# Kernel tuning notes

Hardware: AMD Instinct MI355X
Metric: run time of the kernel (lower is better)

Reference implementation:

```python
import jax, jax.numpy as jnp
import numpy as np

EPS_F = 1e-12
M, N = 64, 4096  # feature dim m, num nodes n


def setup_inputs() -> dict:
    key = jax.random.key(0)
    k1, k2, k3, k4 = jax.random.split(key, 4)
    # X: (m, n) node features transposed, as in the repo (features.t())
    X = jax.random.normal(k1, (M, N), dtype=jnp.float32)
    # F: (m, m) parameter, xavier_uniform init
    bound = float(np.sqrt(6.0 / (M + M)))
    F = jax.random.uniform(k2, (M, M), minval=-bound, maxval=bound, dtype=jnp.float32)
    # Q_S: (n, n) orthogonal eigenvector matrix of the (symmetric, normalized) adjacency
    A = jax.random.normal(k3, (N, N), dtype=jnp.float32)
    Q_S, _ = jnp.linalg.qr(A)
    Q_S = Q_S.astype(jnp.float32)
    # Lambda_S: (n, 1) eigenvalues of normalized adjacency, inside (-1, 1)
    Lambda_S = jnp.sort(
        jax.random.uniform(k4, (N, 1), minval=-0.95, maxval=0.95, dtype=jnp.float32), axis=0
    )
    gamma = jnp.asarray(0.8, dtype=jnp.float32)
    return {"X": X, "F": F, "Q_S": Q_S, "Lambda_S": Lambda_S, "gamma": gamma}


def reference(X, F, Q_S, Lambda_S, gamma):
    # g(F) = F^T F / (||F^T F||_F + eps)  -- Frobenius-normalized Gram matrix
    FF = F.T @ F                                   # (m, m)
    G_F = FF / (jnp.linalg.norm(FF) + EPS_F)       # (m, m), symmetric PSD, ||.||_F ~ 1
    # spectral decomposition of g(F)
    Lambda_F, Q_F = jnp.linalg.eigh(G_F)           # (m,), (m, m)
    # closed-form equilibrium of Z = gamma * g(F) Z S^T + X in the joint eigenbasis
    D = 1.0 / (1.0 - gamma * Lambda_F[:, None] * Lambda_S.reshape(1, -1))  # (m, n)
    Z = Q_F @ (D * (Q_F.T @ X @ Q_S)) @ Q_S.T      # (m, n)
    return Z
```

## Files before the change

### kernel.cpp

```cpp
#include <hip/hip_runtime.h>
#include <math.h>


typedef short short8 __attribute__((ext_vector_type(8)));
typedef float floatx16 __attribute__((ext_vector_type(16)));

#define KSPLIT 16
#define KCHUNK 256
constexpr int Mdim = 64;
constexpr int Ndim = 4096;

__device__ inline ushort f2bf(float f) {
    uint u = __float_as_uint(f);
    u += 0x7fff + ((u >> 16) & 1);
    return (ushort)(u >> 16);
}
__device__ inline float bf2f(ushort h) { return __uint_as_float(((uint)h) << 16); }

__device__ inline floatx16 mfma_bf16(short8 a, short8 b, floatx16 c) {
    return __builtin_amdgcn_mfma_f32_32x32x16_bf16(a, b, c, 0, 0, 0);
}

struct SharedGemm { ushort Ah[4096], Al[4096], Bh[4096]; };
struct SharedPrep { float Fraw[64 * 65]; ushort Ph[4096], Pl[4096]; float red[256]; };
union SharedU { SharedGemm g; SharedPrep p; };

__global__ __launch_bounds__(256) void init_kernel(float* __restrict__ W, float* __restrict__ Z) {
    const int i = blockIdx.x * 256 + threadIdx.x;
    float4 z = {0.f, 0.f, 0.f, 0.f};
    if (i < 65536) *(float4*)&W[i * 4] = z;
    else *(float4*)&Z[(i - 65536) * 4] = z;
}

__device__ void prep_body(SharedPrep& sp, const float* __restrict__ F, float* __restrict__ Gout) {
    const int t = threadIdx.x;
    const int l = t & 63, w = t >> 6;
    const int tm = w & 1, tn = w >> 1;
    const int am = tm * 32 + (l & 31);
    const int bn = tn * 32 + (l & 31);
    const int lk = l >> 5;

    for (int s = 0; s < 4; ++s) {
        int e = t + 256 * s;
        int r = e >> 4, q = (e & 15) * 4;
        float4 v = *(const float4*)&F[r * 64 + q];
        float fa[4] = {v.x, v.y, v.z, v.w};
        for (int i = 0; i < 4; ++i) sp.Fraw[r * 65 + q + i] = fa[i];
    }
    __syncthreads();
    {
        int c = t >> 2, kbase = (t & 3) * 16;
        ushort hh[16], ll[16];
#pragma unroll
        for (int kk = 0; kk < 16; ++kk) {
            float v = sp.Fraw[(kbase + kk) * 65 + c];
            ushort h = f2bf(v);
            hh[kk] = h;
            ll[kk] = f2bf(v - bf2f(h));
        }
#pragma unroll
        for (int g = 0; g < 2; ++g) {
            int gk = (kbase >> 3) + g;
            int idx = c * 64 + ((gk ^ (c & 7)) * 8);
#pragma unroll
            for (int u = 0; u < 8; ++u) { sp.Ph[idx + u] = hh[8 * g + u]; sp.Pl[idx + u] = ll[8 * g + u]; }
        }
    }
    __syncthreads();
    floatx16 acc;
    for (int i = 0; i < 16; ++i) acc[i] = 0.f;
    for (int s16 = 0; s16 < 4; ++s16) {
        int gk = 2 * s16 + lk;
        int ai = am * 64 + ((gk ^ (am & 7)) * 8);
        int bi = bn * 64 + ((gk ^ (bn & 7)) * 8);
        short8 ah = *(const short8*)&sp.Ph[ai];
        short8 al = *(const short8*)&sp.Pl[ai];
        short8 bh = *(const short8*)&sp.Ph[bi];
        short8 bl = *(const short8*)&sp.Pl[bi];
        acc = mfma_bf16(ah, bh, acc);
        acc = mfma_bf16(al, bh, acc);
        acc = mfma_bf16(ah, bl, acc);
    }
    float ss = 0.f;
    for (int r = 0; r < 16; ++r) ss += acc[r] * acc[r];
    sp.red[t] = ss;
    __syncthreads();
    for (int off = 128; off > 0; off >>= 1) {
        if (t < off) sp.red[t] += sp.red[t + off];
        __syncthreads();
    }
    const float inv = 1.0f / (sqrtf(sp.red[0]) + 1e-12f);
    for (int r = 0; r < 16; ++r) {
        int row = (r & 3) + 8 * (r >> 2) + 4 * lk + tm * 32;
        int col = tn * 32 + (l & 31);
        float v = acc[r] * inv;
        Gout[row * 64 + col] = v;
        ushort h = f2bf(v);
        int idx = row * 64 + (((col >> 3) ^ (row & 7)) * 8 + (col & 7));
        sp.Ph[idx] = h;
        sp.Pl[idx] = f2bf(v - bf2f(h));
    }
    for (int j = 1; j < 5; ++j) {
        __syncthreads();
        floatx16 a2;
        for (int i = 0; i < 16; ++i) a2[i] = 0.f;
        for (int s16 = 0; s16 < 4; ++s16) {
            int gk = 2 * s16 + lk;
            int ai = am * 64 + ((gk ^ (am & 7)) * 8);
            int bi = bn * 64 + ((gk ^ (bn & 7)) * 8);
            short8 ah = *(const short8*)&sp.Ph[ai];
            short8 al = *(const short8*)&sp.Pl[ai];
            short8 bh = *(const short8*)&sp.Ph[bi];
            short8 bl = *(const short8*)&sp.Pl[bi];
            a2 = mfma_bf16(ah, bh, a2);
            a2 = mfma_bf16(al, bh, a2);
            a2 = mfma_bf16(ah, bl, a2);
        }
        __syncthreads();
        for (int r = 0; r < 16; ++r) {
            int row = (r & 3) + 8 * (r >> 2) + 4 * lk + tm * 32;
            int col = tn * 32 + (l & 31);
            float v = a2[r];
            Gout[j * 4096 + row * 64 + col] = v;
            ushort h = f2bf(v);
            int idx = row * 64 + (((col >> 3) ^ (row & 7)) * 8 + (col & 7));
            sp.Ph[idx] = h;
            sp.Pl[idx] = f2bf(v - bf2f(h));
        }
    }
}

template <bool TB, bool DOPREP>
__global__ __launch_bounds__(256, 4) void gemm_kernel(const float* __restrict__ A,
                                                      const float* __restrict__ Bm,
                                                      float* __restrict__ C,
                                                      const float* __restrict__ F,
                                                      float* __restrict__ Gp) {
    __shared__ SharedU sh;
    const int bid = blockIdx.x;
    if (DOPREP) {
        if (bid == 0) { prep_body(sh.p, F, Gp); return; }
    }
    const int b = DOPREP ? bid - 1 : bid;
    const int n0 = (b & 63) * 64;
    const int kb = (b >> 6) * KCHUNK;
    const int t = threadIdx.x;
    const int l = t & 63, w = t >> 6;
    const int tm = w & 1, tn = w >> 1;
    const int am = tm * 32 + (l & 31);
    const int bn = tn * 32 + (l & 31);
    const int lk = l >> 5;
    const int sr = t >> 2, sj = t & 3;
    const int nq = t & 15, kr2 = 2 * (t >> 4);

    floatx16 acc;
    for (int i = 0; i < 16; ++i) acc[i] = 0.f;

    float4 bbuf[2][4];
    if (TB) {
#pragma unroll
        for (int s = 0; s < 4; ++s)
            bbuf[0][s] = *(const float4*)&Bm[(size_t)(n0 + sr) * 4096 + kb + 4 * sj + 16 * s];
    } else {
#pragma unroll
        for (int s = 0; s < 2; ++s) {
            bbuf[0][2 * s + 0] = *(const float4*)&Bm[(size_t)(kb + kr2 + 32 * s) * 4096 + n0 + 4 * nq];
            bbuf[0][2 * s + 1] = *(const float4*)&Bm[(size_t)(kb + kr2 + 1 + 32 * s) * 4096 + n0 + 4 * nq];
        }
    }

#pragma unroll
    for (int step = 0; step < KCHUNK / 64; ++step) {
        const int k0 = kb + step * 64;
        const int cur = step & 1, nxt = cur ^ 1;
        float4 av[4];
#pragma unroll
        for (int s = 0; s < 4; ++s)
            av[s] = *(const float4*)&A[sr * 4096 + k0 + 4 * sj + 16 * s];
        __syncthreads();
        if (step + 1 < KCHUNK / 64) {
            const int k1 = k0 + 64;
            if (TB) {
#pragma unroll
                for (int s = 0; s < 4; ++s)
                    bbuf[nxt][s] = *(const float4*)&Bm[(size_t)(n0 + sr) * 4096 + k1 + 4 * sj + 16 * s];
            } else {
#pragma unroll
                for (int s = 0; s < 2; ++s) {
                    bbuf[nxt][2 * s + 0] = *(const float4*)&Bm[(size_t)(k1 + kr2 + 32 * s) * 4096 + n0 + 4 * nq];
                    bbuf[nxt][2 * s + 1] = *(const float4*)&Bm[(size_t)(k1 + kr2 + 1 + 32 * s) * 4096 + n0 + 4 * nq];
                }
            }
        }
        if (TB) {
#pragma unroll
            for (int s = 0; s < 4; ++s) {
                int off = 4 * sj + 16 * s;
                int idx = sr * 64 + (((off >> 3) ^ (sr & 7)) * 8 + (off & 7));
                float fb[4] = {bbuf[cur][s].x, bbuf[cur][s].y, bbuf[cur][s].z, bbuf[cur][s].w};
                ushort4 h4;
                ushort* hp = (ushort*)&h4;
#pragma unroll
                for (int i = 0; i < 4; ++i) hp[i] = f2bf(fb[i]);
                *(ushort4*)&sh.g.Bh[idx] = h4;
            }
        } else {
#pragma unroll
            for (int s = 0; s < 2; ++s) {
                int k = kr2 + 32 * s;
                float fa[4] = {bbuf[cur][2 * s].x, bbuf[cur][2 * s].y, bbuf[cur][2 * s].z, bbuf[cur][2 * s].w};
                float fb[4] = {bbuf[cur][2 * s + 1].x, bbuf[cur][2 * s + 1].y, bbuf[cur][2 * s + 1].z, bbuf[cur][2 * s + 1].w};
#pragma unroll
                for (int i = 0; i < 4; ++i) {
                    int n = 4 * nq + i;
                    int idx = n * 64 + (((k >> 3) ^ (n & 7)) * 8 + (k & 7));
                    ushort2 hp2;
                    hp2.x = f2bf(fa[i]);
                    hp2.y = f2bf(fb[i]);
                    *(ushort2*)&sh.g.Bh[idx] = hp2;
                }
            }
        }
#pragma unroll
        for (int s = 0; s < 4; ++s) {
            int off = 4 * sj + 16 * s;
            int idx = sr * 64 + (((off >> 3) ^ (sr & 7)) * 8 + (off & 7));
            float fa[4] = {av[s].x, av[s].y, av[s].z, av[s].w};
            ushort4 h4, l4;
            ushort* hp = (ushort*)&h4; ushort* lp = (ushort*)&l4;
#pragma unroll
            for (int i = 0; i < 4; ++i) {
                ushort h = f2bf(fa[i]);
                hp[i] = h; lp[i] = f2bf(fa[i] - bf2f(h));
            }
            *(ushort4*)&sh.g.Ah[idx] = h4;
            *(ushort4*)&sh.g.Al[idx] = l4;
        }
        __syncthreads();
#pragma unroll
        for (int s16 = 0; s16 < 4; ++s16) {
            int gk = 2 * s16 + lk;
            int ai = am * 64 + ((gk ^ (am & 7)) * 8);
            int bi = bn * 64 + ((gk ^ (bn & 7)) * 8);
            short8 ah = *(const short8*)&sh.g.Ah[ai];
            short8 al = *(const short8*)&sh.g.Al[ai];
            short8 bh = *(const short8*)&sh.g.Bh[bi];
            acc = mfma_bf16(ah, bh, acc);
            acc = mfma_bf16(al, bh, acc);
        }
    }
    const int colg = n0 + tn * 32 + (l & 31);
#pragma unroll
    for (int r = 0; r < 16; ++r) {
        int row = (r & 3) + 8 * (r >> 2) + 4 * lk + tm * 32;
        atomicAdd(&C[row * 4096 + colg], acc[r]);
    }
}

__global__ __launch_bounds__(256) void solve_kernel(const float* __restrict__ W,
                                                    const float* __restrict__ Gp,
                                                    const float* __restrict__ lam,
                                                    const float* __restrict__ gammap,
                                                    float* __restrict__ Y) {
    __shared__ float Gs[64][68];
    __shared__ float T[64][17];
    const int t = threadIdx.x;
    const int c0 = blockIdx.x * 16;
    for (int e = t; e < 1024; e += 256)
        T[e >> 4][e & 15] = W[(e >> 4) * 4096 + c0 + (e & 15)];
    const int tx = t & 15;
    const int r4 = (t >> 4) * 4;
    const float a = gammap[0] * lam[c0 + tx];
    float s = a;
    for (int j = 0; j < 5; ++j) {
        __syncthreads();
        for (int e = t; e < 4096; e += 256) Gs[e >> 6][e & 63] = Gp[j * 4096 + e];
        __syncthreads();
        float u0 = 0.f, u1 = 0.f, u2 = 0.f, u3 = 0.f;
#pragma unroll 8
        for (int k = 0; k < 64; ++k) {
            const float tv = T[k][tx];
            const float4 g = *(const float4*)&Gs[k][r4];
            u0 += g.x * tv; u1 += g.y * tv; u2 += g.z * tv; u3 += g.w * tv;
        }
        __syncthreads();
        T[r4 + 0][tx] += s * u0;
        T[r4 + 1][tx] += s * u1;
        T[r4 + 2][tx] += s * u2;
        T[r4 + 3][tx] += s * u3;
        s = s * s;
    }
    __syncthreads();
    for (int e = t; e < 1024; e += 256)
        Y[(e >> 4) * 4096 + c0 + (e & 15)] = T[e >> 4][e & 15];
}

extern "C" void kernel_launch(void* const* d_in, const int* in_sizes, int n_in,
                              void* d_out, int out_size, void* d_ws, size_t ws_size,
                              hipStream_t stream) {
    const float* X     = (const float*)d_in[0];
    const float* F     = (const float*)d_in[1];
    const float* Qs    = (const float*)d_in[2];
    const float* lam   = (const float*)d_in[3];
    const float* gamma = (const float*)d_in[4];
    float* Z = (float*)d_out;

    float* W  = (float*)d_ws;
    float* Y  = W + Mdim * Ndim;
    float* Gp = Y + Mdim * Ndim;

    init_kernel<<<512, 256, 0, stream>>>(W, Z);
    gemm_kernel<false, true><<<64 * KSPLIT + 1, 256, 0, stream>>>(X, Qs, W, F, Gp);
    solve_kernel<<<Ndim / 16, 256, 0, stream>>>(W, Gp, lam, gamma, Y);
    gemm_kernel<true, false><<<64 * KSPLIT, 256, 0, stream>>>(Y, Qs, Z, nullptr, nullptr);
}
```

Before: 158.1 us.

## Shrink GEMM LDS footprint, double K-split, use barriers without vmem drain

The prep block now reuses the GEMM shared buffers instead of a larger union, which cuts per-block LDS and lets the launch bound ask for 6 blocks per SM. The K chunk is halved and the split doubled, so twice as many blocks launch with fewer steps each. __syncthreads is replaced by a barrier that waits only on LDS counters, so global prefetch loads stay in flight across the barrier. The trade-offs are more atomicAdd traffic into the output and more register pressure.

```diff
diff --git a/kernel.cpp b/kernel.cpp
--- a/kernel.cpp
+++ b/kernel.cpp
@@ -5,8 +5,8 @@
 typedef short short8 __attribute__((ext_vector_type(8)));
 typedef float floatx16 __attribute__((ext_vector_type(16)));
 
-#define KSPLIT 16
-#define KCHUNK 256
+#define KSPLIT 32
+#define KCHUNK 128
 constexpr int Mdim = 64;
 constexpr int Ndim = 4096;
 
@@ -22,8 +22,12 @@
 }
 
 struct SharedGemm { ushort Ah[4096], Al[4096], Bh[4096]; };
-struct SharedPrep { float Fraw[64 * 65]; ushort Ph[4096], Pl[4096]; float red[256]; };
-union SharedU { SharedGemm g; SharedPrep p; };
+
+__device__ inline void barrier_nodrain() {
+    asm volatile("s_waitcnt lgkmcnt(0)" ::: "memory");
+    __builtin_amdgcn_s_barrier();
+    __builtin_amdgcn_sched_barrier(0);
+}
 
 __global__ __launch_bounds__(256) void init_kernel(float* __restrict__ W, float* __restrict__ Z) {
     const int i = blockIdx.x * 256 + threadIdx.x;
@@ -32,38 +36,29 @@
     else *(float4*)&Z[(i - 65536) * 4] = z;
 }
 
-__device__ void prep_body(SharedPrep& sp, const float* __restrict__ F, float* __restrict__ Gout) {
+__device__ void prep_body(SharedGemm& sg, const float* __restrict__ F, float* __restrict__ Gout) {
     const int t = threadIdx.x;
     const int l = t & 63, w = t >> 6;
     const int tm = w & 1, tn = w >> 1;
     const int am = tm * 32 + (l & 31);
     const int bn = tn * 32 + (l & 31);
     const int lk = l >> 5;
-
-    for (int s = 0; s < 4; ++s) {
-        int e = t + 256 * s;
-        int r = e >> 4, q = (e & 15) * 4;
-        float4 v = *(const float4*)&F[r * 64 + q];
-        float fa[4] = {v.x, v.y, v.z, v.w};
-        for (int i = 0; i < 4; ++i) sp.Fraw[r * 65 + q + i] = fa[i];
-    }
-    __syncthreads();
+    float* red = (float*)sg.Bh;
+
     {
-        int c = t >> 2, kbase = (t & 3) * 16;
-        ushort hh[16], ll[16];
-#pragma unroll
-        for (int kk = 0; kk < 16; ++kk) {
-            float v = sp.Fraw[(kbase + kk) * 65 + c];
-            ushort h = f2bf(v);
-            hh[kk] = h;
-            ll[kk] = f2bf(v - bf2f(h));
-        }
-#pragma unroll
-        for (int g = 0; g < 2; ++g) {
-            int gk = (kbase >> 3) + g;
-            int idx = c * 64 + ((gk ^ (c & 7)) * 8);
-#pragma unroll
-            for (int u = 0; u < 8; ++u) { sp.Ph[idx + u] = hh[8 * g + u]; sp.Pl[idx + u] = ll[8 * g + u]; }
+        const int r = t >> 2, c0 = (t & 3) * 16;
+#pragma unroll
+        for (int q = 0; q < 4; ++q) {
+            float4 v = *(const float4*)&F[r * 64 + c0 + 4 * q];
+            float fa[4] = {v.x, v.y, v.z, v.w};
+#pragma unroll
+            for (int i = 0; i < 4; ++i) {
+                int c = c0 + 4 * q + i;
+                ushort h = f2bf(fa[i]);
+                int idx = c * 64 + (((r >> 3) ^ (c & 7)) * 8) + (r & 7);
+                sg.Ah[idx] = h;
+                sg.Al[idx] = f2bf(fa[i] - bf2f(h));
+            }
         }
     }
     __syncthreads();
@@ -73,23 +68,23 @@
         int gk = 2 * s16 + lk;
         int ai = am * 64 + ((gk ^ (am & 7)) * 8);
         int bi = bn * 64 + ((gk ^ (bn & 7)) * 8);
-        short8 ah = *(const short8*)&sp.Ph[ai];
-        short8 al = *(const short8*)&sp.Pl[ai];
-        short8 bh = *(const short8*)&sp.Ph[bi];
-        short8 bl = *(const short8*)&sp.Pl[bi];
+        short8 ah = *(const short8*)&sg.Ah[ai];
+        short8 al = *(const short8*)&sg.Al[ai];
+        short8 bh = *(const short8*)&sg.Ah[bi];
+        short8 bl = *(const short8*)&sg.Al[bi];
         acc = mfma_bf16(ah, bh, acc);
         acc = mfma_bf16(al, bh, acc);
         acc = mfma_bf16(ah, bl, acc);
     }
     float ss = 0.f;
     for (int r = 0; r < 16; ++r) ss += acc[r] * acc[r];
-    sp.red[t] = ss;
+    red[t] = ss;
     __syncthreads();
     for (int off = 128; off > 0; off >>= 1) {
-        if (t < off) sp.red[t] += sp.red[t + off];
-        __syncthreads();
-    }
-    const float inv = 1.0f / (sqrtf(sp.red[0]) + 1e-12f);
+        if (t < off) red[t] += red[t + off];
+        __syncthreads();
+    }
+    const float inv = 1.0f / (sqrtf(red[0]) + 1e-12f);
     for (int r = 0; r < 16; ++r) {
         int row = (r & 3) + 8 * (r >> 2) + 4 * lk + tm * 32;
         int col = tn * 32 + (l & 31);
@@ -97,8 +92,8 @@
         Gout[row * 64 + col] = v;
         ushort h = f2bf(v);
         int idx = row * 64 + (((col >> 3) ^ (row & 7)) * 8 + (col & 7));
-        sp.Ph[idx] = h;
-        sp.Pl[idx] = f2bf(v - bf2f(h));
+        sg.Ah[idx] = h;
+        sg.Al[idx] = f2bf(v - bf2f(h));
     }
     for (int j = 1; j < 5; ++j) {
         __syncthreads();
@@ -108,10 +103,10 @@
             int gk = 2 * s16 + lk;
             int ai = am * 64 + ((gk ^ (am & 7)) * 8);
             int bi = bn * 64 + ((gk ^ (bn & 7)) * 8);
-            short8 ah = *(const short8*)&sp.Ph[ai];
-            short8 al = *(const short8*)&sp.Pl[ai];
-            short8 bh = *(const short8*)&sp.Ph[bi];
-            short8 bl = *(const short8*)&sp.Pl[bi];
+            short8 ah = *(const short8*)&sg.Ah[ai];
+            short8 al = *(const short8*)&sg.Al[ai];
+            short8 bh = *(const short8*)&sg.Ah[bi];
+            short8 bl = *(const short8*)&sg.Al[bi];
             a2 = mfma_bf16(ah, bh, a2);
             a2 = mfma_bf16(al, bh, a2);
             a2 = mfma_bf16(ah, bl, a2);
@@ -124,22 +119,22 @@
             Gout[j * 4096 + row * 64 + col] = v;
             ushort h = f2bf(v);
             int idx = row * 64 + (((col >> 3) ^ (row & 7)) * 8 + (col & 7));
-            sp.Ph[idx] = h;
-            sp.Pl[idx] = f2bf(v - bf2f(h));
+            sg.Ah[idx] = h;
+            sg.Al[idx] = f2bf(v - bf2f(h));
         }
     }
 }
 
 template <bool TB, bool DOPREP>
-__global__ __launch_bounds__(256, 4) void gemm_kernel(const float* __restrict__ A,
+__global__ __launch_bounds__(256, 6) void gemm_kernel(const float* __restrict__ A,
                                                       const float* __restrict__ Bm,
                                                       float* __restrict__ C,
                                                       const float* __restrict__ F,
                                                       float* __restrict__ Gp) {
-    __shared__ SharedU sh;
+    __shared__ SharedGemm sh;
     const int bid = blockIdx.x;
     if (DOPREP) {
-        if (bid == 0) { prep_body(sh.p, F, Gp); return; }
+        if (bid == 0) { prep_body(sh, F, Gp); return; }
     }
     const int b = DOPREP ? bid - 1 : bid;
     const int n0 = (b & 63) * 64;
@@ -177,7 +172,6 @@
 #pragma unroll
         for (int s = 0; s < 4; ++s)
             av[s] = *(const float4*)&A[sr * 4096 + k0 + 4 * sj + 16 * s];
-        __syncthreads();
         if (step + 1 < KCHUNK / 64) {
             const int k1 = k0 + 64;
             if (TB) {
@@ -192,6 +186,7 @@
                 }
             }
         }
+        barrier_nodrain();
         if (TB) {
 #pragma unroll
             for (int s = 0; s < 4; ++s) {
@@ -202,7 +197,7 @@
                 ushort* hp = (ushort*)&h4;
 #pragma unroll
                 for (int i = 0; i < 4; ++i) hp[i] = f2bf(fb[i]);
-                *(ushort4*)&sh.g.Bh[idx] = h4;
+                *(ushort4*)&sh.Bh[idx] = h4;
             }
         } else {
 #pragma unroll
@@ -217,7 +212,7 @@
                     ushort2 hp2;
                     hp2.x = f2bf(fa[i]);
                     hp2.y = f2bf(fb[i]);
-                    *(ushort2*)&sh.g.Bh[idx] = hp2;
+                    *(ushort2*)&sh.Bh[idx] = hp2;
                 }
             }
         }
@@ -233,18 +228,18 @@
                 ushort h = f2bf(fa[i]);
                 hp[i] = h; lp[i] = f2bf(fa[i] - bf2f(h));
             }
-            *(ushort4*)&sh.g.Ah[idx] = h4;
-            *(ushort4*)&sh.g.Al[idx] = l4;
-        }
-        __syncthreads();
+            *(ushort4*)&sh.Ah[idx] = h4;
+            *(ushort4*)&sh.Al[idx] = l4;
+        }
+        barrier_nodrain();
 #pragma unroll
         for (int s16 = 0; s16 < 4; ++s16) {
             int gk = 2 * s16 + lk;
             int ai = am * 64 + ((gk ^ (am & 7)) * 8);
             int bi = bn * 64 + ((gk ^ (bn & 7)) * 8);
-            short8 ah = *(const short8*)&sh.g.Ah[ai];
-            short8 al = *(const short8*)&sh.g.Al[ai];
-            short8 bh = *(const short8*)&sh.g.Bh[bi];
+            short8 ah = *(const short8*)&sh.Ah[ai];
+            short8 al = *(const short8*)&sh.Al[ai];
+            short8 bh = *(const short8*)&sh.Bh[bi];
             acc = mfma_bf16(ah, bh, acc);
             acc = mfma_bf16(al, bh, acc);
         }
```

Measured after the change: 173.4 us. 1.1x slower.
